# Performance work log

Hardware: AMD Instinct MI355X
Metric: run time of the kernel (lower is better)

Reference implementation:

```python
import jax, jax.numpy as jnp
import numpy as np

DIM = 1024
NH = 8
HD = DIM // NH  # 128
E = 8
EPS = 1e-5


def rope_cos_sin(L, hd):
    # matches RotaryPositionEmbedding: emb = cat([freqs, freqs], -1)
    inv_freq = 1.0 / (10000.0 ** (jnp.arange(0, hd, 2, dtype=jnp.float32) / hd))
    freqs = jnp.arange(L, dtype=jnp.float32)[:, None] * inv_freq[None, :]  # (L, hd/2)
    emb = jnp.concatenate([freqs, freqs], axis=-1)  # (L, hd)
    return jnp.cos(emb), jnp.sin(emb)


def rotate_half(x):
    # interleaved rotate, as in the torch apply_rope
    x1 = x[..., 0::2]
    x2 = x[..., 1::2]
    return jnp.stack((-x2, x1), axis=-1).reshape(x.shape)


def rope(t, cos, sin):
    # t: (B,H,L,D); cos/sin: (L,D)
    return t * cos[None, None] + rotate_half(t) * sin[None, None]


def heads(t):
    B, L, C = t.shape
    return t.reshape(B, L, NH, HD).transpose(0, 2, 1, 3)  # (B,H,L,D)


def setup_inputs() -> dict:
    key = jax.random.key(0)
    ks = jax.random.split(key, 32)
    std = 0.02
    d = {}
    d['x'] = jax.random.normal(ks[0], (16, 512, DIM), jnp.float32)
    d['h_a'] = jax.random.normal(ks[1], (16, 256, DIM), jnp.float32)
    d['h_t'] = jax.random.normal(ks[2], (16, 256, DIM), jnp.float32)
    names = ['qa', 'ka', 'va', 'qt', 'kt', 'vt', 'o', 'ffn']
    for i, n in enumerate(names):
        d['W_' + n] = jax.random.normal(ks[3 + 2 * i], (E, DIM, DIM), jnp.float32) * std
        d['b_' + n] = jax.random.normal(ks[4 + 2 * i], (E, DIM), jnp.float32) * std
    d['gamma'] = jnp.ones((E, DIM), jnp.float32)
    d['beta'] = jnp.zeros((E, DIM), jnp.float32)
    d['gating_factor'] = jnp.zeros((E,), jnp.float32)
    d['expert_idx'] = 3
    return d


def reference(x, h_a, h_t,
              W_qa, b_qa, W_ka, b_ka, W_va, b_va,
              W_qt, b_qt, W_kt, b_kt, W_vt, b_vt,
              W_o, b_o, W_ffn, b_ffn,
              gamma, beta, gating_factor, expert_idx):
    e = expert_idx

    def lin(t, W, b):
        return t @ W[e].T + b[e]

    B, T, C = x.shape
    Ka = h_a.shape[1]
    Kt = h_t.shape[1]

    q_a = heads(lin(x, W_qa, b_qa))        # (B,H,T,D)
    q_t = heads(lin(x, W_qt, b_qt))
    k_a = heads(lin(h_a, W_ka, b_ka))      # (B,H,Ka,D)
    v_a = heads(lin(h_a, W_va, b_va))
    k_t = heads(lin(h_t, W_kt, b_kt))      # (B,H,Kt,D)
    v_t = heads(lin(h_t, W_vt, b_vt))

    cos_m, sin_m = rope_cos_sin(T, HD)
    q_a = rope(q_a, cos_m, sin_m)
    q_t = rope(q_t, cos_m, sin_m)
    cos_a, sin_a = rope_cos_sin(Ka, HD)
    k_a = rope(k_a, cos_a, sin_a)
    cos_t, sin_t = rope_cos_sin(Kt, HD)
    k_t = rope(k_t, cos_t, sin_t)

    ratio_g = jax.nn.sigmoid(gating_factor[e])
    s_a = jnp.einsum('bhtd,bhkd->bhtk', q_a, k_a)
    s_t = jnp.einsum('bhtd,bhkd->bhtk', q_t, k_t) * ratio_g
    scores = jnp.concatenate([s_a, s_t], axis=-1) / np.sqrt(HD)
    w = jax.nn.softmax(scores, axis=-1)            # (B,H,T,Ka+Kt)
    v = jnp.concatenate([v_a, v_t], axis=2)        # (B,H,Ka+Kt,D)
    out = jnp.einsum('bhtk,bhkd->bhtd', w, v)
    out = out.transpose(0, 2, 1, 3).reshape(B, T, C)
    out = lin(out, W_o, b_o)

    x = out + x
    # ffn: SmileMoENorm -> SmileMoELinear -> ReLU (no extra residual)
    mu = jnp.mean(x, axis=-1, keepdims=True)
    var = jnp.var(x, axis=-1, keepdims=True)
    xn = (x - mu) / jnp.sqrt(var + EPS) * gamma[e] + beta[e]
    x = jax.nn.relu(lin(xn, W_ffn, b_ffn))
    return x
```

## Files before the change

### kernel.cpp

```cpp
#include <hip/hip_runtime.h>
#include <stdint.h>

typedef __bf16 bf16x8 __attribute__((ext_vector_type(8)));
typedef float f32x4 __attribute__((ext_vector_type(4)));
typedef unsigned short u16x8 __attribute__((ext_vector_type(8)));

typedef const __attribute__((address_space(1))) void* gas_ptr;
typedef __attribute__((address_space(3))) void* las_ptr;
typedef const __attribute__((address_space(3))) char* lds_c3;

__device__ __forceinline__ void gload16(const void* g, void* l) {
  __builtin_amdgcn_global_load_lds((gas_ptr)g, (las_ptr)l, 16, 0, 0);
}

__device__ __forceinline__ bf16x8 dsread16(const char* p) {
  bf16x8 r;
  asm volatile("ds_read_b128 %0, %1" : "=v"(r) : "v"((lds_c3)p));
  return r;
}
__device__ __forceinline__ void dswrite2(char* p, uint32_t v) {
  asm volatile("ds_write_b16 %0, %1" : : "v"((las_ptr)p), "v"(v));
}
template <int OFF>
__device__ __forceinline__ float dswz(float x) {
  float r;
  asm volatile("ds_swizzle_b32 %0, %1 offset:%c2" : "=v"(r) : "v"(x), "i"(OFF));
  return r;
}

__device__ __forceinline__ unsigned short f2bf(float f) {
  uint32_t u = __float_as_uint(f);
  u += 0x7FFFu + ((u >> 16) & 1u);
  return (unsigned short)(u >> 16);
}
__device__ __forceinline__ float bf2f(unsigned short u) {
  return __uint_as_float(((uint32_t)u) << 16);
}

#define SB __builtin_amdgcn_sched_barrier(0)
#define BAR __builtin_amdgcn_s_barrier()
#define LGK0 asm volatile("s_waitcnt lgkmcnt(0)")

__device__ __forceinline__ void conv8(const float* __restrict__ src,
                                      unsigned short* __restrict__ dst, int i) {
  const float4* s4 = (const float4*)src;
  float4 a = s4[2 * i], b = s4[2 * i + 1];
  u16x8 r;
  r[0] = f2bf(a.x); r[1] = f2bf(a.y); r[2] = f2bf(a.z); r[3] = f2bf(a.w);
  r[4] = f2bf(b.x); r[5] = f2bf(b.y); r[6] = f2bf(b.z); r[7] = f2bf(b.w);
  *(u16x8*)&dst[(size_t)i * 8] = r;
}

__global__ __launch_bounds__(256)
void prep_all(const float* __restrict__ x, const float* __restrict__ h_a,
              const float* __restrict__ h_t,
              const float* W0, const float* W1, const float* W2, const float* W3,
              const float* W4, const float* W5, const float* W6, const float* W7,
              const int* __restrict__ eptr,
              unsigned short* __restrict__ XB, unsigned short* __restrict__ HAB,
              unsigned short* __restrict__ HTB, unsigned short* __restrict__ WW,
              float* __restrict__ cosb, float* __restrict__ sinb) {
  const int blk = blockIdx.x, tid = threadIdx.x;
  if (blk < 4096) {
    conv8(x, XB, blk * 256 + tid);
  } else if (blk < 6144) {
    conv8(h_a, HAB, (blk - 4096) * 256 + tid);
  } else if (blk < 8192) {
    conv8(h_t, HTB, (blk - 6144) * 256 + tid);
  } else if (blk < 12288) {
    const int w = (blk - 8192) >> 9;
    const int i = ((blk - 8192) & 511) * 256 + tid;
    const float* wp;
    switch (w) {
      case 0: wp = W0; break; case 1: wp = W1; break;
      case 2: wp = W2; break; case 3: wp = W3; break;
      case 4: wp = W4; break; case 5: wp = W5; break;
      case 6: wp = W6; break; default: wp = W7; break;
    }
    conv8(wp + (size_t)(*eptr) * 1048576, WW + (size_t)w * 1048576, i);
  } else {
    const int i = (blk - 12288) * 256 + tid;
    const int t = i >> 7, d = i & 127;
    const int f = d & 63;
    float invf = expf(-0.14391156831212787f * (float)f);
    float ang = (float)t * invf;
    float s, c;
    sincosf(ang, &s, &c);
    cosb[i] = c;
    sinb[i] = s;
  }
}

template <int MODE>
__global__ __launch_bounds__(512, 1)
void gemm3r(const unsigned short* __restrict__ A0, const unsigned short* __restrict__ A1,
            const unsigned short* __restrict__ W0, const unsigned short* __restrict__ W1,
            const unsigned short* __restrict__ W2, const unsigned short* __restrict__ W3,
            const float* __restrict__ bias0, const float* __restrict__ bias1,
            const float* __restrict__ bias2, const float* __restrict__ bias3,
            const int* __restrict__ eptr, const float* __restrict__ ctab,
            const float* __restrict__ stab,
            unsigned short* __restrict__ out0, unsigned short* __restrict__ out1,
            unsigned short* __restrict__ outV,
            const float* __restrict__ resid, unsigned short* __restrict__ outbf,
            float* __restrict__ outf) {
  __shared__ __align__(16) char AL[98304];
  __shared__ __align__(16) char BL[49152];
  const int tid = threadIdx.x;
  const int lane = tid & 63, wid = tid >> 6, fr = lane & 15, g = lane >> 4;
  const int wm = wid >> 1, wn = wid & 1;
  const int id = blockIdx.x;
  constexpr int CPX = (MODE == 0) ? 64 : 32;
  const int swz = (id & 7) * CPX + (id >> 3);
  constexpr int NBNS = (MODE <= 1) ? 4 : 3;
  const int bm = swz >> NBNS;
  const int bn = swz & ((1 << NBNS) - 1);
  const int z = (MODE == 1) ? blockIdx.y : 0;
  const int e = *eptr;

  const unsigned short* Asel;
  const unsigned short* Wsel;
  const float* bias;
  int half = 0, cb0;
  if constexpr (MODE == 0) {
    Asel = A0;
    half = bn >> 3;
    Wsel = half ? W1 : W0;
    bias = (half ? bias1 : bias0) + e * 1024;
    cb0 = (bn & 7) * 128;
  } else if constexpr (MODE == 1) {
    Asel = z ? A1 : A0;
    half = bn >> 3;
    Wsel = z ? (half ? W3 : W2) : (half ? W1 : W0);
    bias = (z ? (half ? bias3 : bias2) : (half ? bias1 : bias0)) + e * 1024;
    cb0 = (bn & 7) * 128;
  } else {
    Asel = A0;
    Wsel = W0;
    bias = bias0 + e * 1024;
    cb0 = bn * 128;
  }

  const char* Ab = (const char*)Asel + (size_t)bm * 256 * 2048;
  const char* Bb = (const char*)Wsel + (size_t)cb0 * 2048;

  const int csw = (((tid & 7) ^ ((tid >> 3) & 7)) << 4);
  const char* Ags = Ab + (tid >> 3) * 2048 + csw;
  const char* Bgs = Bb + (tid >> 3) * 2048 + csw;
  char* Ald = AL + tid * 16;
  char* Bld = BL + tid * 16;

#define STA(T, BUF)                                                         \
  { const char* s_ = Ags + (T) * 128;                                       \
    char* d_ = Ald + (BUF) * 32768;                                         \
    gload16(s_, d_);                  gload16(s_ + 131072, d_ + 8192);      \
    gload16(s_ + 262144, d_ + 16384); gload16(s_ + 393216, d_ + 24576); }
#define STB(T, BUF)                                                         \
  { const char* s_ = Bgs + (T) * 128;                                       \
    char* d_ = Bld + (BUF) * 16384;                                         \
    gload16(s_, d_);                  gload16(s_ + 131072, d_ + 8192); }

  const int lsw7 = fr & 7;
  const int ksel = (wid & 4) ? 4 : 0;
  const int cA = ((ksel + g) ^ lsw7) << 4;
  const int cB = (((4 - ksel) + g) ^ lsw7) << 4;
  const int arow = (wm * 64 + fr) * 128;
  const int brow = (wn * 64 + fr) * 128;

  f32x4 acc[4][4];
#pragma unroll
  for (int m = 0; m < 4; ++m)
#pragma unroll
    for (int n = 0; n < 4; ++n) acc[m][n] = f32x4{0.f, 0.f, 0.f, 0.f};
  bf16x8 af[4], bf[4];

#define RDAB(BASEA, BASEB, C)                                               \
  { const char* pa_ = (BASEA) + arow + (C);                                 \
    const char* pb_ = (BASEB) + brow + (C);                                 \
    _Pragma("unroll") for (int m = 0; m < 4; ++m)                           \
        af[m] = dsread16(pa_ + m * 2048);                                   \
    _Pragma("unroll") for (int n = 0; n < 4; ++n)                           \
        bf[n] = dsread16(pb_ + n * 2048); }

#define MF16                                                                \
  __builtin_amdgcn_s_setprio(1);                                            \
  _Pragma("unroll") for (int m = 0; m < 4; ++m)                             \
    _Pragma("unroll") for (int n = 0; n < 4; ++n)                           \
        acc[m][n] = __builtin_amdgcn_mfma_f32_16x16x32_bf16(                \
            af[m], bf[n], acc[m][n], 0, 0, 0);                              \
  __builtin_amdgcn_s_setprio(0);

  STA(0, 0); STB(0, 0); STA(1, 1); STB(1, 1);

  int bc = 0;
#pragma unroll 1
  for (int t = 0; t < 16; ++t) {
    SB;
    if (t <= 14) asm volatile("s_waitcnt vmcnt(6)");
    else         asm volatile("s_waitcnt vmcnt(0)");
    BAR; SB;
    const char* ALc = AL + bc * 32768;
    const char* BLc = BL + bc * 16384;
    const int bs = bc ? bc - 1 : 2;
    RDAB(ALc, BLc, cA); SB;
    if (t <= 13) STA(t + 2, bs);
    SB; LGK0; SB;
    MF16 SB;
    RDAB(ALc, BLc, cB); SB;
    if (t <= 13) STB(t + 2, bs);
    SB; LGK0; SB;
    MF16 SB;
    bc = (bc == 2) ? 0 : bc + 1;
  }
#undef RDAB
#undef MF16
#undef STA
#undef STB

  const int wrow0 = bm * 256 + wm * 64;
#pragma unroll
  for (int m = 0; m < 4; ++m) {
#pragma unroll
    for (int n = 0; n < 4; ++n) {
      const int lc = wn * 64 + n * 16 + fr;
      const int gc = cb0 + lc;
      const float bv = bias[gc];
#pragma unroll
      for (int j = 0; j < 4; ++j) {
        const int grow = wrow0 + m * 16 + g * 4 + j;
        float v = acc[m][n][j] + bv;
        if constexpr (MODE == 0) {
          const int t = grow & 511, bb = grow >> 9;
          const int hh = gc >> 7, dd = gc & 127;
          float pv = __shfl_xor(v, 1);
          float cs = ctab[t * 128 + dd], sn = stab[t * 128 + dd];
          float rh = (dd & 1) ? pv : -pv;
          float o = v * cs + rh * sn;
          unsigned short* dst = half ? out1 : out0;
          dst[(((size_t)(bb * 8 + hh) * 512 + t) << 7) + dd] = f2bf(o);
        } else if constexpr (MODE == 1) {
          const int t = grow & 255, bb = grow >> 8;
          const int hh = gc >> 7, dd = gc & 127;
          if (half == 0) {
            float pv = __shfl_xor(v, 1);
            float cs = ctab[t * 128 + dd], sn = stab[t * 128 + dd];
            float rh = (dd & 1) ? pv : -pv;
            float o = v * cs + rh * sn;
            unsigned short* dst = z ? out1 : out0;
            dst[(((size_t)(bb * 8 + hh) * 256 + t) << 7) + dd] = f2bf(o);
          } else {
            outV[(((size_t)(bb * 8 + hh) << 7) + dd) * 512 + z * 256 + t] = f2bf(v);
          }
        } else if constexpr (MODE == 2) {
          const size_t idx = ((size_t)grow << 10) + gc;
          outbf[idx] = f2bf(v + resid[idx]);
        } else {
          const size_t idx = ((size_t)grow << 10) + gc;
          outf[idx] = fmaxf(v, 0.f);
        }
      }
    }
  }
}

__global__ __launch_bounds__(256, 2)
void attn_kernel(const unsigned short* __restrict__ QA, const unsigned short* __restrict__ QT,
                 const unsigned short* __restrict__ KA, const unsigned short* __restrict__ KT,
                 const unsigned short* __restrict__ VT,
                 unsigned short* __restrict__ AO,
                 const float* __restrict__ gating, const int* __restrict__ eptr) {
  __shared__ unsigned short Ks[2][8192];
  __shared__ unsigned short Vs[2][8192];
  __shared__ unsigned short Ps[8192];
  const int tid = threadIdx.x, lane = tid & 63, wv = tid >> 6;
  const int fr = lane & 15, g = lane >> 4;
  const int id = blockIdx.x;
  const int bid = (id & 7) * 64 + (id >> 3);
  const int b = bid >> 5, h = (bid >> 2) & 7, q0 = (bid & 3) << 7;
  const float ratio = 1.f / (1.f + __expf(-gating[*eptr]));
  const float SC = 0.08838834764831845f;
  const size_t bh = (size_t)(b * 8 + h);

  bf16x8 qf[2][4];
  {
    const char* qa = (const char*)QA + ((bh * 512 + q0 + wv * 32 + fr) << 8) + g * 16;
#pragma unroll
    for (int mb = 0; mb < 2; ++mb)
#pragma unroll
      for (int kb = 0; kb < 4; ++kb)
        qf[mb][kb] = *(const bf16x8*)(qa + mb * 4096 + kb * 64);
  }

  auto stage = [&](int t, int buf) {
    const char* kgb = (const char*)((t < 4) ? KA : KT) + ((bh * 256 + ((size_t)(t & 3) << 6)) << 8);
    const char* vgb = (const char*)VT + (bh << 17) + (t << 7);
    char* ksd = (char*)Ks[buf] + tid * 16;
    char* vsd = (char*)Vs[buf] + tid * 16;
#pragma unroll
    for (int j = 0; j < 4; ++j) {
      const int rk = j * 16 + (tid >> 4);
      const int ck = ((tid & 15) << 4) ^ ((rk & 7) << 4);
      gload16(kgb + rk * 256 + ck, ksd + j * 4096);
      const int dv = j * 32 + (tid >> 3);
      const int cv = ((tid & 7) << 4) ^ ((dv & 7) << 4);
      gload16(vgb + dv * 1024 + cv, vsd + j * 4096);
    }
  };

  float m_run[2][4], l_run[2][4];
  f32x4 oacc[2][8];
#pragma unroll
  for (int mb = 0; mb < 2; ++mb) {
#pragma unroll
    for (int j = 0; j < 4; ++j) { m_run[mb][j] = -1e30f; l_run[mb][j] = 0.f; }
#pragma unroll
    for (int db = 0; db < 8; ++db) oacc[mb][db] = f32x4{0.f, 0.f, 0.f, 0.f};
  }

  stage(0, 0);

  for (int it = 0; it < 8; ++it) {
    const int cur = it & 1;
    if (it < 7) stage(it + 1, cur ^ 1);
    SB;
    if (it < 7) asm volatile("s_waitcnt vmcnt(8)");
    else        asm volatile("s_waitcnt vmcnt(0)");
    SB;
    BAR;
    SB;

    if (it == 4) {
      const char* qt = (const char*)QT + ((bh * 512 + q0 + wv * 32 + fr) << 8) + g * 16;
#pragma unroll
      for (int mb = 0; mb < 2; ++mb)
#pragma unroll
        for (int kb = 0; kb < 4; ++kb)
          qf[mb][kb] = *(const bf16x8*)(qt + mb * 4096 + kb * 64);
    }
    const float sc = (it < 4) ? SC : SC * ratio;
    const char* kc = (const char*)Ks[cur];
    const char* vc = (const char*)Vs[cur];

    f32x4 s[2][4];
#pragma unroll
    for (int mb = 0; mb < 2; ++mb)
#pragma unroll
      for (int nb = 0; nb < 4; ++nb) s[mb][nb] = f32x4{0.f, 0.f, 0.f, 0.f};
    bf16x8 kfa[4], kfb[4];
#pragma unroll
    for (int kb = 0; kb < 4; ++kb) {
      const int byt = (fr * 256 + kb * 64 + g * 16) ^ ((fr & 7) << 4);
      kfa[kb] = dsread16(kc + byt);
    }
#pragma unroll
    for (int nb = 0; nb < 4; ++nb) {
      if (nb < 3) {
#pragma unroll
        for (int kb = 0; kb < 4; ++kb) {
          const int r = (nb + 1) * 16 + fr;
          const int byt = (r * 256 + kb * 64 + g * 16) ^ ((r & 7) << 4);
          if (nb & 1) kfa[kb] = dsread16(kc + byt);
          else        kfb[kb] = dsread16(kc + byt);
        }
        asm volatile("s_waitcnt lgkmcnt(4)");
      } else {
        asm volatile("s_waitcnt lgkmcnt(0)");
      }
      SB;
      __builtin_amdgcn_s_setprio(1);
#pragma unroll
      for (int kb = 0; kb < 4; ++kb) {
        bf16x8 kf = (nb & 1) ? kfb[kb] : kfa[kb];
        s[0][nb] = __builtin_amdgcn_mfma_f32_16x16x32_bf16(qf[0][kb], kf, s[0][nb], 0, 0, 0);
        s[1][nb] = __builtin_amdgcn_mfma_f32_16x16x32_bf16(qf[1][kb], kf, s[1][nb], 0, 0, 0);
      }
      __builtin_amdgcn_s_setprio(0);
    }
    SB;

    float red[8];
#pragma unroll
    for (int mb = 0; mb < 2; ++mb)
#pragma unroll
      for (int j = 0; j < 4; ++j) {
        float mx = -1e30f;
#pragma unroll
        for (int nb = 0; nb < 4; ++nb) {
          s[mb][nb][j] *= sc;
          mx = fmaxf(mx, s[mb][nb][j]);
        }
        red[mb * 4 + j] = mx;
      }
#define MAXR(OFF)                                                        \
    { float tmp[8];                                                      \
      _Pragma("unroll") for (int k = 0; k < 8; ++k) tmp[k] = dswz<OFF>(red[k]); \
      asm volatile("s_waitcnt lgkmcnt(0)");                              \
      SB;                                                                \
      _Pragma("unroll") for (int k = 0; k < 8; ++k) red[k] = fmaxf(red[k], tmp[k]); }
    MAXR(0x041F) MAXR(0x081F) MAXR(0x101F) MAXR(0x201F)
#undef MAXR
#pragma unroll
    for (int mb = 0; mb < 2; ++mb)
#pragma unroll
      for (int j = 0; j < 4; ++j) {
        const float mn = fmaxf(m_run[mb][j], red[mb * 4 + j]);
        const float alpha = __expf(m_run[mb][j] - mn);
        m_run[mb][j] = mn;
        l_run[mb][j] *= alpha;
#pragma unroll
        for (int db = 0; db < 8; ++db) oacc[mb][db][j] *= alpha;
      }
#pragma unroll
    for (int mb = 0; mb < 2; ++mb)
#pragma unroll
      for (int nb = 0; nb < 4; ++nb)
#pragma unroll
        for (int j = 0; j < 4; ++j) {
          float p = __expf(s[mb][nb][j] - m_run[mb][j]);
          l_run[mb][j] += p;
          const int r = wv * 32 + mb * 16 + g * 4 + j;
          const int byt = (r * 128 + (nb * 16 + fr) * 2) ^ ((r & 7) << 4);
          dswrite2((char*)Ps + byt, (uint32_t)f2bf(p));
        }

#pragma unroll
    for (int kb2 = 0; kb2 < 2; ++kb2) {
      bf16x8 pf[2], vf[8];
#pragma unroll
      for (int mb = 0; mb < 2; ++mb) {
        const int r = wv * 32 + mb * 16 + fr;
        const int byt = (r * 128 + kb2 * 64 + g * 16) ^ ((r & 7) << 4);
        pf[mb] = dsread16((const char*)Ps + byt);
      }
#pragma unroll
      for (int db = 0; db < 8; ++db) {
        const int rv = db * 16 + fr;
        const int byt = (rv * 128 + kb2 * 64 + g * 16) ^ ((rv & 7) << 4);
        vf[db] = dsread16(vc + byt);
      }
      asm volatile("s_waitcnt lgkmcnt(0)");
      SB;
      __builtin_amdgcn_s_setprio(1);
#pragma unroll
      for (int db = 0; db < 8; ++db) {
        oacc[0][db] = __builtin_amdgcn_mfma_f32_16x16x32_bf16(pf[0], vf[db], oacc[0][db], 0, 0, 0);
        oacc[1][db] = __builtin_amdgcn_mfma_f32_16x16x32_bf16(pf[1], vf[db], oacc[1][db], 0, 0, 0);
      }
      __builtin_amdgcn_s_setprio(0);
    }
    SB;
    BAR;
  }

#pragma unroll
  for (int mb = 0; mb < 2; ++mb)
#pragma unroll
    for (int j = 0; j < 4; ++j) {
      float lt = l_run[mb][j];
#pragma unroll
      for (int d = 1; d < 16; d <<= 1) lt += __shfl_xor(lt, d);
      float inv = 1.f / lt;
#pragma unroll
      for (int db = 0; db < 8; ++db) {
        float o = oacc[mb][db][j] * inv;
        int row = q0 + wv * 32 + mb * 16 + g * 4 + j;
        int col = h * 128 + db * 16 + fr;
        AO[(((size_t)b * 512 + row) << 10) + col] = f2bf(o);
      }
    }
}

__global__ __launch_bounds__(256)
void ln_kernel(const unsigned short* __restrict__ X2, const float* __restrict__ gbase,
               const float* __restrict__ bbase, const int* __restrict__ eptr,
               unsigned short* __restrict__ XN) {
  const int row = blockIdx.x, tid = threadIdx.x;
  const unsigned short* x = X2 + ((size_t)row << 10);
  ushort4 raw = ((const ushort4*)x)[tid];
  float v0 = bf2f(raw.x), v1 = bf2f(raw.y), v2 = bf2f(raw.z), v3 = bf2f(raw.w);
  float s = v0 + v1 + v2 + v3;
  float ss = v0 * v0 + v1 * v1 + v2 * v2 + v3 * v3;
#pragma unroll
  for (int d = 1; d < 64; d <<= 1) {
    s += __shfl_xor(s, d);
    ss += __shfl_xor(ss, d);
  }
  __shared__ float red[8];
  const int wv = tid >> 6, lane = tid & 63;
  if (lane == 0) { red[wv] = s; red[4 + wv] = ss; }
  __syncthreads();
  s = red[0] + red[1] + red[2] + red[3];
  ss = red[4] + red[5] + red[6] + red[7];
  const float mu = s * 0.0009765625f;
  const float var = ss * 0.0009765625f - mu * mu;
  const float inv = rsqrtf(var + 1e-5f);
  const int e = *eptr;
  const float* gg = gbase + e * 1024 + tid * 4;
  const float* bb = bbase + e * 1024 + tid * 4;
  ushort4 o;
  o.x = f2bf((v0 - mu) * inv * gg[0] + bb[0]);
  o.y = f2bf((v1 - mu) * inv * gg[1] + bb[1]);
  o.z = f2bf((v2 - mu) * inv * gg[2] + bb[2]);
  o.w = f2bf((v3 - mu) * inv * gg[3] + bb[3]);
  *(ushort4*)&XN[((size_t)row << 10) + tid * 4] = o;
}

extern "C" void kernel_launch(void* const* d_in, const int* in_sizes, int n_in,
                              void* d_out, int out_size, void* d_ws, size_t ws_size,
                              hipStream_t stream) {
  (void)in_sizes; (void)n_in; (void)out_size; (void)ws_size;
  const float* x      = (const float*)d_in[0];
  const float* h_a    = (const float*)d_in[1];
  const float* h_t    = (const float*)d_in[2];
  const float* W_qa   = (const float*)d_in[3];
  const float* b_qa   = (const float*)d_in[4];
  const float* W_ka   = (const float*)d_in[5];
  const float* b_ka   = (const float*)d_in[6];
  const float* W_va   = (const float*)d_in[7];
  const float* b_va   = (const float*)d_in[8];
  const float* W_qt   = (const float*)d_in[9];
  const float* b_qt   = (const float*)d_in[10];
  const float* W_kt   = (const float*)d_in[11];
  const float* b_kt   = (const float*)d_in[12];
  const float* W_vt   = (const float*)d_in[13];
  const float* b_vt   = (const float*)d_in[14];
  const float* W_o    = (const float*)d_in[15];
  const float* b_o    = (const float*)d_in[16];
  const float* W_ffn  = (const float*)d_in[17];
  const float* b_ffn  = (const float*)d_in[18];
  const float* gamma  = (const float*)d_in[19];
  const float* beta   = (const float*)d_in[20];
  const float* gating = (const float*)d_in[21];
  const int*   eptr   = (const int*)d_in[22];

  char* ws = (char*)d_ws;
  unsigned short* XB  = (unsigned short*)(ws + 0);
  unsigned short* HAB = (unsigned short*)(ws + 16777216);
  unsigned short* HTB = (unsigned short*)(ws + 25165824);
  unsigned short* X2b = (unsigned short*)(ws + 0);
  unsigned short* WW  = (unsigned short*)(ws + 33554432);
  unsigned short* QAb = (unsigned short*)(ws + 50331648);
  unsigned short* XN  = QAb;
  unsigned short* QTb = (unsigned short*)(ws + 67108864);
  unsigned short* KAb = (unsigned short*)(ws + 83886080);
  unsigned short* KTb = (unsigned short*)(ws + 92274688);
  unsigned short* VTb = (unsigned short*)(ws + 100663296);
  unsigned short* AOb = (unsigned short*)(ws + 117440512);
  float* COS = (float*)(ws + 134217728);
  float* SIN = (float*)(ws + 134479872);

  prep_all<<<12544, 256, 0, stream>>>(x, h_a, h_t,
      W_qa, W_ka, W_va, W_qt, W_kt, W_vt, W_o, W_ffn, eptr,
      XB, HAB, HTB, WW, COS, SIN);

  gemm3r<0><<<dim3(512), 512, 0, stream>>>(XB, nullptr,
      WW + 0ull * 1048576, WW + 3ull * 1048576, nullptr, nullptr,
      b_qa, b_qt, nullptr, nullptr, eptr, COS, SIN,
      QAb, QTb, nullptr, nullptr, nullptr, nullptr);

  gemm3r<1><<<dim3(256, 2), 512, 0, stream>>>(HAB, HTB,
      WW + 1ull * 1048576, WW + 2ull * 1048576,
      WW + 4ull * 1048576, WW + 5ull * 1048576,
      b_ka, b_va, b_kt, b_vt, eptr, COS, SIN,
      KAb, KTb, VTb, nullptr, nullptr, nullptr);

  attn_kernel<<<512, 256, 0, stream>>>(QAb, QTb, KAb, KTb, VTb, AOb, gating, eptr);

  gemm3r<2><<<dim3(256), 512, 0, stream>>>(AOb, nullptr,
      WW + 6ull * 1048576, nullptr, nullptr, nullptr,
      b_o, nullptr, nullptr, nullptr, eptr, nullptr, nullptr,
      nullptr, nullptr, nullptr, x, X2b, nullptr);

  ln_kernel<<<8192, 256, 0, stream>>>(X2b, gamma, beta, eptr, XN);

  gemm3r<3><<<dim3(256), 512, 0, stream>>>(XN, nullptr,
      WW + 7ull * 1048576, nullptr, nullptr, nullptr,
      b_ffn, nullptr, nullptr, nullptr, eptr, nullptr, nullptr,
      nullptr, nullptr, nullptr, nullptr, nullptr, (float*)d_out);
}
```

Measured before the change: 214.9 us.

## Replace Q-projection GEMM with smaller-tile kernel running two blocks per CU

After: 215.3 us. Within noise of the previous version (+0.2%).

```diff
diff --git a/kernel.cpp b/kernel.cpp
--- a/kernel.cpp
+++ b/kernel.cpp
@@ -91,6 +91,125 @@
   }
 }
 
+__global__ __launch_bounds__(512, 2)
+void gemm2b(const unsigned short* __restrict__ A,
+            const unsigned short* __restrict__ W0, const unsigned short* __restrict__ W1,
+            const float* __restrict__ bias0, const float* __restrict__ bias1,
+            const int* __restrict__ eptr, const float* __restrict__ ctab,
+            const float* __restrict__ stab,
+            unsigned short* __restrict__ out0, unsigned short* __restrict__ out1) {
+  __shared__ __align__(16) char AL[32768];
+  __shared__ __align__(16) char BL[32768];
+  const int tid = threadIdx.x;
+  const int lane = tid & 63, wid = tid >> 6, fr = lane & 15, g = lane >> 4;
+  const int wm = wid >> 2, wn = wid & 3;
+  const int id = blockIdx.x;
+  const int swz = (id & 7) * 128 + (id >> 3);
+  const int bm = swz >> 4, bn = swz & 15;
+  const int e = *eptr;
+  const int half = bn >> 3;
+  const int cb0 = (bn & 7) * 128;
+  const unsigned short* Wsel = half ? W1 : W0;
+  const float* bias = (half ? bias1 : bias0) + e * 1024;
+
+  const char* Ab = (const char*)A + (size_t)bm * 128 * 2048;
+  const char* Bb = (const char*)Wsel + (size_t)cb0 * 2048;
+
+  const int csw = (((tid & 7) ^ ((tid >> 3) & 7)) << 4);
+  const char* Ags = Ab + (tid >> 3) * 2048 + csw;
+  const char* Bgs = Bb + (tid >> 3) * 2048 + csw;
+  char* Ald = AL + tid * 16;
+  char* Bld = BL + tid * 16;
+
+#define STA2(T, BUF)                                             \
+  { const char* s_ = Ags + (T) * 128;                            \
+    char* d_ = Ald + (BUF) * 16384;                              \
+    gload16(s_, d_); gload16(s_ + 131072, d_ + 8192); }
+#define STB2(T, BUF)                                             \
+  { const char* s_ = Bgs + (T) * 128;                            \
+    char* d_ = Bld + (BUF) * 16384;                              \
+    gload16(s_, d_); gload16(s_ + 131072, d_ + 8192); }
+
+  const int lsw7 = fr & 7;
+  const int ksel = (wid & 4) ? 4 : 0;
+  const int cA = ((ksel + g) ^ lsw7) << 4;
+  const int cB = (((4 - ksel) + g) ^ lsw7) << 4;
+
+  f32x4 acc[4][2];
+#pragma unroll
+  for (int m = 0; m < 4; ++m)
+#pragma unroll
+    for (int n = 0; n < 2; ++n) acc[m][n] = f32x4{0.f, 0.f, 0.f, 0.f};
+  bf16x8 af1[4], bf1[2], af2[4], bf2[2];
+
+#define RD6(BASEA, BASEB, C, AF, BF)                                        \
+  { const char* pa_ = (BASEA) + (wm * 64 + fr) * 128 + (C);                 \
+    const char* pb_ = (BASEB) + (wn * 32 + fr) * 128 + (C);                 \
+    _Pragma("unroll") for (int m = 0; m < 4; ++m)                           \
+        AF[m] = dsread16(pa_ + m * 2048);                                   \
+    _Pragma("unroll") for (int n = 0; n < 2; ++n)                           \
+        BF[n] = dsread16(pb_ + n * 2048); }
+
+#define MF8(AF, BF)                                                         \
+  __builtin_amdgcn_s_setprio(1);                                            \
+  _Pragma("unroll") for (int m = 0; m < 4; ++m)                             \
+    _Pragma("unroll") for (int n = 0; n < 2; ++n)                           \
+        acc[m][n] = __builtin_amdgcn_mfma_f32_16x16x32_bf16(                \
+            AF[m], BF[n], acc[m][n], 0, 0, 0);                              \
+  __builtin_amdgcn_s_setprio(0);
+
+  STA2(0, 0); STB2(0, 0); STA2(1, 1); STB2(1, 1);
+
+#pragma unroll 1
+  for (int t = 0; t < 16; ++t) {
+    SB;
+    if (t <= 14) asm volatile("s_waitcnt vmcnt(4)");
+    else         asm volatile("s_waitcnt vmcnt(0)");
+    BAR; SB;
+    const int buf = t & 1;
+    const char* ALc = AL + buf * 16384;
+    const char* BLc = BL + buf * 16384;
+    RD6(ALc, BLc, cA, af1, bf1);
+    RD6(ALc, BLc, cB, af2, bf2);
+    SB;
+    asm volatile("s_waitcnt lgkmcnt(6)");
+    SB;
+    MF8(af1, bf1) SB;
+    LGK0;
+    BAR; SB;
+    if (t <= 13) { STA2(t + 2, buf); STB2(t + 2, buf); }
+    SB;
+    MF8(af2, bf2) SB;
+  }
+#undef RD6
+#undef MF8
+#undef STA2
+#undef STB2
+
+  const int wrow0 = bm * 128 + wm * 64;
+#pragma unroll
+  for (int m = 0; m < 4; ++m) {
+#pragma unroll
+    for (int n = 0; n < 2; ++n) {
+      const int gc = cb0 + wn * 32 + n * 16 + fr;
+      const float bv = bias[gc];
+#pragma unroll
+      for (int j = 0; j < 4; ++j) {
+        const int grow = wrow0 + m * 16 + g * 4 + j;
+        float v = acc[m][n][j] + bv;
+        const int t = grow & 511, bb = grow >> 9;
+        const int hh = gc >> 7, dd = gc & 127;
+        float pv = __shfl_xor(v, 1);
+        float cs = ctab[t * 128 + dd], sn = stab[t * 128 + dd];
+        float rh = (dd & 1) ? pv : -pv;
+        float o = v * cs + rh * sn;
+        unsigned short* dst = half ? out1 : out0;
+        dst[(((size_t)(bb * 8 + hh) * 512 + t) << 7) + dd] = f2bf(o);
+      }
+    }
+  }
+}
+
 template <int MODE>
 __global__ __launch_bounds__(512, 1)
 void gemm3r(const unsigned short* __restrict__ A0, const unsigned short* __restrict__ A1,
@@ -110,9 +229,8 @@
   const int lane = tid & 63, wid = tid >> 6, fr = lane & 15, g = lane >> 4;
   const int wm = wid >> 1, wn = wid & 1;
   const int id = blockIdx.x;
-  constexpr int CPX = (MODE == 0) ? 64 : 32;
-  const int swz = (id & 7) * CPX + (id >> 3);
-  constexpr int NBNS = (MODE <= 1) ? 4 : 3;
+  const int swz = (id & 7) * 32 + (id >> 3);
+  constexpr int NBNS = (MODE == 1) ? 4 : 3;
   const int bm = swz >> NBNS;
   const int bn = swz & ((1 << NBNS) - 1);
   const int z = (MODE == 1) ? blockIdx.y : 0;
@@ -122,13 +240,7 @@
   const unsigned short* Wsel;
   const float* bias;
   int half = 0, cb0;
-  if constexpr (MODE == 0) {
-    Asel = A0;
-    half = bn >> 3;
-    Wsel = half ? W1 : W0;
-    bias = (half ? bias1 : bias0) + e * 1024;
-    cb0 = (bn & 7) * 128;
-  } else if constexpr (MODE == 1) {
+  if constexpr (MODE == 1) {
     Asel = z ? A1 : A0;
     half = bn >> 3;
     Wsel = z ? (half ? W3 : W2) : (half ? W1 : W0);
@@ -229,16 +341,7 @@
       for (int j = 0; j < 4; ++j) {
         const int grow = wrow0 + m * 16 + g * 4 + j;
         float v = acc[m][n][j] + bv;
-        if constexpr (MODE == 0) {
-          const int t = grow & 511, bb = grow >> 9;
-          const int hh = gc >> 7, dd = gc & 127;
-          float pv = __shfl_xor(v, 1);
-          float cs = ctab[t * 128 + dd], sn = stab[t * 128 + dd];
-          float rh = (dd & 1) ? pv : -pv;
-          float o = v * cs + rh * sn;
-          unsigned short* dst = half ? out1 : out0;
-          dst[(((size_t)(bb * 8 + hh) * 512 + t) << 7) + dd] = f2bf(o);
-        } else if constexpr (MODE == 1) {
+        if constexpr (MODE == 1) {
           const int t = grow & 255, bb = grow >> 8;
           const int hh = gc >> 7, dd = gc & 127;
           if (half == 0) {
@@ -553,10 +656,9 @@
       W_qa, W_ka, W_va, W_qt, W_kt, W_vt, W_o, W_ffn, eptr,
       XB, HAB, HTB, WW, COS, SIN);
 
-  gemm3r<0><<<dim3(512), 512, 0, stream>>>(XB, nullptr,
-      WW + 0ull * 1048576, WW + 3ull * 1048576, nullptr, nullptr,
-      b_qa, b_qt, nullptr, nullptr, eptr, COS, SIN,
-      QAb, QTb, nullptr, nullptr, nullptr, nullptr);
+  gemm2b<<<dim3(1024), 512, 0, stream>>>(XB,
+      WW + 0ull * 1048576, WW + 3ull * 1048576,
+      b_qa, b_qt, eptr, COS, SIN, QAb, QTb);
 
   gemm3r<1><<<dim3(256, 2), 512, 0, stream>>>(HAB, HTB,
       WW + 1ull * 1048576, WW + 2ull * 1048576,
```
